# Optimization experiments

Hardware: AMD Instinct MI355X
Metric: run time of the kernel (lower is better)

Reference implementation:

```python
import jax, jax.numpy as jnp
import numpy as np


def setup_inputs() -> dict:
    key = jax.random.key(0)
    k1, k2 = jax.random.split(key)
    x = jax.random.normal(k1, (8, 64, 224, 224), dtype=jnp.float32)
    kernel = jax.random.normal(k2, (64, 1, 3, 3), dtype=jnp.float32)
    return {"x": x, "kernel": kernel, "stride": 1, "padding": 1, "dilation": 1}


def reference(x, kernel, stride, padding, dilation):
    # Tropical-max (morphological dilation) conv: out[b,c,i,j] =
    #   max_{ki,kj} x_pad[b,c,i*stride+ki*dilation, j*stride+kj*dilation] + kernel[c,0,ki,kj]
    # Padding uses the tropical neutral element -inf, matching the torch module.
    B, C, H, W = x.shape
    O, _, K, _ = kernel.shape
    out_h = (H + 2 * padding - dilation * (K - 1) - 1) // stride + 1
    out_w = (W + 2 * padding - dilation * (K - 1) - 1) // stride + 1
    neutral = -jnp.inf
    xp = jnp.pad(x, ((0, 0), (0, 0), (padding, padding), (padding, padding)),
                 constant_values=neutral)
    # Initialize at -inf: equivalent to the module's extra neutral pad on the K axis.
    acc = jnp.full((B, C, out_h, out_w), neutral, dtype=x.dtype)
    h_span = (out_h - 1) * stride + 1
    w_span = (out_w - 1) * stride + 1
    # Small fixed K*K loop over kernel taps; avoids materializing the unfolded tensor.
    for ki in range(K):
        for kj in range(K):
            patch = jax.lax.slice(
                xp,
                (0, 0, ki * dilation, kj * dilation),
                (B, C, ki * dilation + h_span, kj * dilation + w_span),
                (1, 1, stride, stride),
            )  # [B, C, out_h, out_w]
            acc = jnp.maximum(acc, patch + kernel[None, :, 0, ki, kj, None, None])
    return acc
```

## Files before the change

kernel.cpp:

```cpp
#include <hip/hip_runtime.h>
#include <math.h>


#define H_DIM 224
#define W_DIM 224
#define W4 56
#define G4 56
#define C_DIM 64

__global__ __launch_bounds__(256) void tropical_conv_kernel(
    const float* __restrict__ x,
    const float* __restrict__ kern,
    float* __restrict__ out,
    int total)
{
    int idx = blockIdx.x * blockDim.x + threadIdx.x;
    if (idx >= total) return;

    const float NEG = -INFINITY;

    int j4 = idx % W4;
    int t  = idx / W4;
    int g  = t % G4;
    int bc = t / G4;
    int c  = bc & (C_DIM - 1);

    const float* kc = kern + c * 9;
    float k00 = kc[0], k01 = kc[1], k02 = kc[2];
    float k10 = kc[3], k11 = kc[4], k12 = kc[5];
    float k20 = kc[6], k21 = kc[7], k22 = kc[8];

    const float* plane = x + (size_t)bc * (H_DIM * W_DIM);
    int j0 = j4 * 4;
    int i0 = g * 4;

    float4 rv[6];
    float  lf[6], rg[6];
    #pragma unroll
    for (int rr = 0; rr < 6; ++rr) {
        int r = i0 - 1 + rr;
        if (r >= 0 && r < H_DIM) {
            const float* row = plane + r * W_DIM;
            rv[rr] = *(const float4*)(row + j0);
            lf[rr] = (j4 > 0)      ? row[j0 - 1] : NEG;
            rg[rr] = (j4 < W4 - 1) ? row[j0 + 4] : NEG;
        } else {
            rv[rr] = make_float4(NEG, NEG, NEG, NEG);
            lf[rr] = NEG;
            rg[rr] = NEG;
        }
    }

    float* oplane = out + (size_t)bc * (H_DIM * W_DIM);

    #pragma unroll
    for (int o = 0; o < 4; ++o) {
        float4 acc = make_float4(NEG, NEG, NEG, NEG);
        #pragma unroll
        for (int ki = 0; ki < 3; ++ki) {
            int rr = o + ki;
            float t0 = (ki == 0) ? k00 : (ki == 1) ? k10 : k20;
            float t1 = (ki == 0) ? k01 : (ki == 1) ? k11 : k21;
            float t2 = (ki == 0) ? k02 : (ki == 1) ? k12 : k22;
            float4 a = rv[rr];
            acc.x = fmaxf(acc.x, fmaxf(fmaxf(lf[rr] + t0, a.x + t1), a.y   + t2));
            acc.y = fmaxf(acc.y, fmaxf(fmaxf(a.x   + t0, a.y + t1), a.z   + t2));
            acc.z = fmaxf(acc.z, fmaxf(fmaxf(a.y   + t0, a.z + t1), a.w   + t2));
            acc.w = fmaxf(acc.w, fmaxf(fmaxf(a.z   + t0, a.w + t1), rg[rr] + t2));
        }
        *(float4*)(oplane + (size_t)(i0 + o) * W_DIM + j0) = acc;
    }
}

extern "C" void kernel_launch(void* const* d_in, const int* in_sizes, int n_in,
                              void* d_out, int out_size, void* d_ws, size_t ws_size,
                              hipStream_t stream) {
    const float* x    = (const float*)d_in[0];
    const float* kern = (const float*)d_in[1];
    float* out        = (float*)d_out;

    const int total = 8 * C_DIM * G4 * W4;
    const int block = 256;
    const int grid  = (total + block - 1) / block;
    tropical_conv_kernel<<<grid, block, 0, stream>>>(x, kern, out, total);
}
```

Before: 183.4 us.

## Widen per-thread tile to 8 columns with branch-free interior loads and nontemporal stores

Each thread now computes a 4x8 output tile instead of 4x4, loading two float4 per row. This cuts the redundant halo loads per output and halves the thread count. Interior strips take a branch-free load path with clamped halo indices, and edge strips clamp row indices. Outputs are written with nontemporal stores, and launch bounds request 2 blocks per SM. The wider tile raises register pressure and makes each warp's accesses less coalesced.

Result: slower. 206.3 us (+12.5%).

```diff
diff --git a/kernel.cpp b/kernel.cpp
--- a/kernel.cpp
+++ b/kernel.cpp
@@ -4,11 +4,19 @@
 
 #define H_DIM 224
 #define W_DIM 224
-#define W4 56
-#define G4 56
+#define W8 28
+#define STRIP 4
+#define GS (H_DIM / STRIP)
 #define C_DIM 64
+#define NEG (-INFINITY)
 
-__global__ __launch_bounds__(256) void tropical_conv_kernel(
+typedef float f4v __attribute__((ext_vector_type(4)));
+
+__device__ __forceinline__ float m3(float a, float b, float c) {
+    return fmaxf(fmaxf(a, b), c);
+}
+
+__global__ __launch_bounds__(256, 2) void tropical_conv_kernel(
     const float* __restrict__ x,
     const float* __restrict__ kern,
     float* __restrict__ out,
@@ -17,12 +25,10 @@
     int idx = blockIdx.x * blockDim.x + threadIdx.x;
     if (idx >= total) return;
 
-    const float NEG = -INFINITY;
-
-    int j4 = idx % W4;
-    int t  = idx / W4;
-    int g  = t % G4;
-    int bc = t / G4;
+    int j8 = idx % W8;
+    int t  = idx / W8;
+    int g  = t % GS;
+    int bc = t / GS;
     int c  = bc & (C_DIM - 1);
 
     const float* kc = kern + c * 9;
@@ -30,45 +36,80 @@
     float k10 = kc[3], k11 = kc[4], k12 = kc[5];
     float k20 = kc[6], k21 = kc[7], k22 = kc[8];
 
-    const float* plane = x + (size_t)bc * (H_DIM * W_DIM);
-    int j0 = j4 * 4;
-    int i0 = g * 4;
+    const float* plane  = x   + (size_t)bc * (H_DIM * W_DIM);
+    float*       oplane = out + (size_t)bc * (H_DIM * W_DIM);
+    int j0 = j8 * 8;
+    int i0 = g * STRIP;
 
-    float4 rv[6];
+    bool has_l = (j8 > 0);
+    bool has_r = (j8 < W8 - 1);
+    int  jl    = has_l ? j0 - 1 : 0;
+    int  jr    = has_r ? j0 + 8 : W_DIM - 1;
+
+    float4 v0[6], v1[6];
     float  lf[6], rg[6];
-    #pragma unroll
-    for (int rr = 0; rr < 6; ++rr) {
-        int r = i0 - 1 + rr;
-        if (r >= 0 && r < H_DIM) {
-            const float* row = plane + r * W_DIM;
-            rv[rr] = *(const float4*)(row + j0);
-            lf[rr] = (j4 > 0)      ? row[j0 - 1] : NEG;
-            rg[rr] = (j4 < W4 - 1) ? row[j0 + 4] : NEG;
-        } else {
-            rv[rr] = make_float4(NEG, NEG, NEG, NEG);
-            lf[rr] = NEG;
-            rg[rr] = NEG;
+
+    if (g > 0 && g < GS - 1) {
+        const float* row = plane + (size_t)(i0 - 1) * W_DIM;
+        #pragma unroll
+        for (int rr = 0; rr < 6; ++rr) {
+            v0[rr] = *(const float4*)(row + j0);
+            v1[rr] = *(const float4*)(row + j0 + 4);
+            lf[rr] = row[jl];
+            rg[rr] = row[jr];
+            row += W_DIM;
+        }
+        #pragma unroll
+        for (int rr = 0; rr < 6; ++rr) {
+            lf[rr] = has_l ? lf[rr] : NEG;
+            rg[rr] = has_r ? rg[rr] : NEG;
+        }
+    } else {
+        #pragma unroll
+        for (int rr = 0; rr < 6; ++rr) {
+            int r  = i0 - 1 + rr;
+            int rc = r < 0 ? 0 : (r >= H_DIM ? H_DIM - 1 : r);
+            const float* row = plane + (size_t)rc * W_DIM;
+            v0[rr] = *(const float4*)(row + j0);
+            v1[rr] = *(const float4*)(row + j0 + 4);
+            lf[rr] = has_l ? row[jl] : NEG;
+            rg[rr] = has_r ? row[jr] : NEG;
+            bool oob = (r < 0) || (r >= H_DIM);
+            if (oob) {
+                v0[rr] = make_float4(NEG, NEG, NEG, NEG);
+                v1[rr] = make_float4(NEG, NEG, NEG, NEG);
+                lf[rr] = NEG;
+                rg[rr] = NEG;
+            }
         }
     }
 
-    float* oplane = out + (size_t)bc * (H_DIM * W_DIM);
+    float X[6][10];
+    #pragma unroll
+    for (int rr = 0; rr < 6; ++rr) {
+        X[rr][0] = lf[rr];
+        X[rr][1] = v0[rr].x; X[rr][2] = v0[rr].y;
+        X[rr][3] = v0[rr].z; X[rr][4] = v0[rr].w;
+        X[rr][5] = v1[rr].x; X[rr][6] = v1[rr].y;
+        X[rr][7] = v1[rr].z; X[rr][8] = v1[rr].w;
+        X[rr][9] = rg[rr];
+    }
 
     #pragma unroll
-    for (int o = 0; o < 4; ++o) {
-        float4 acc = make_float4(NEG, NEG, NEG, NEG);
+    for (int o = 0; o < STRIP; ++o) {
+        float ot[8];
         #pragma unroll
-        for (int ki = 0; ki < 3; ++ki) {
-            int rr = o + ki;
-            float t0 = (ki == 0) ? k00 : (ki == 1) ? k10 : k20;
-            float t1 = (ki == 0) ? k01 : (ki == 1) ? k11 : k21;
-            float t2 = (ki == 0) ? k02 : (ki == 1) ? k12 : k22;
-            float4 a = rv[rr];
-            acc.x = fmaxf(acc.x, fmaxf(fmaxf(lf[rr] + t0, a.x + t1), a.y   + t2));
-            acc.y = fmaxf(acc.y, fmaxf(fmaxf(a.x   + t0, a.y + t1), a.z   + t2));
-            acc.z = fmaxf(acc.z, fmaxf(fmaxf(a.y   + t0, a.z + t1), a.w   + t2));
-            acc.w = fmaxf(acc.w, fmaxf(fmaxf(a.z   + t0, a.w + t1), rg[rr] + t2));
+        for (int ci = 0; ci < 8; ++ci) {
+            float m0 = m3(X[o    ][ci] + k00, X[o    ][ci + 1] + k01, X[o    ][ci + 2] + k02);
+            float m1 = m3(X[o + 1][ci] + k10, X[o + 1][ci + 1] + k11, X[o + 1][ci + 2] + k12);
+            float m2 = m3(X[o + 2][ci] + k20, X[o + 2][ci + 1] + k21, X[o + 2][ci + 2] + k22);
+            ot[ci] = m3(m0, m1, m2);
         }
-        *(float4*)(oplane + (size_t)(i0 + o) * W_DIM + j0) = acc;
+        float* orow = oplane + (size_t)(i0 + o) * W_DIM + j0;
+        f4v s0 = {ot[0], ot[1], ot[2], ot[3]};
+        f4v s1 = {ot[4], ot[5], ot[6], ot[7]};
+        __builtin_nontemporal_store(s0, (f4v*)orow);
+        __builtin_nontemporal_store(s1, (f4v*)(orow + 4));
     }
 }
 
@@ -79,7 +120,7 @@
     const float* kern = (const float*)d_in[1];
     float* out        = (float*)d_out;
 
-    const int total = 8 * C_DIM * G4 * W4;
+    const int total = 8 * C_DIM * GS * W8;
     const int block = 256;
     const int grid  = (total + block - 1) / block;
     tropical_conv_kernel<<<grid, block, 0, stream>>>(x, kern, out, total);
```
